# Optimization experiments

Measured on AMD Instinct MI355X. Metric: run time of the kernel, lower is better.

## Reference

```python
import jax, jax.numpy as jnp
import numpy as np

N, L, D_IN = 8192, 32, 256   # total paths, max path len, token+method embed
E, H, T, C = 128, 128, 128, 2  # encode_size, hidden_dim, test_vector_size, label_count
G = 1024                      # number of methods (groups)
LN_EPS = 1e-5


def _lstm_last_hidden(xs, lengths, Wih, Whh, bih, bhh):
    """Single-layer LSTM over padded [N,L,E]; returns h at t=length-1 per row (packed-sequence h_n)."""
    xs_t = jnp.transpose(xs, (1, 0, 2))  # [L, N, E]
    n = xs.shape[0]
    h0 = jnp.zeros((n, H), xs.dtype)
    c0 = jnp.zeros((n, H), xs.dtype)

    def step(carry, inp):
        h, c = carry
        x_t, t = inp
        gates = x_t @ Wih.T + bih + h @ Whh.T + bhh  # [N, 4H], torch gate order i,f,g,o
        i, f, g, o = jnp.split(gates, 4, axis=-1)
        c_new = jax.nn.sigmoid(f) * c + jax.nn.sigmoid(i) * jnp.tanh(g)
        h_new = jax.nn.sigmoid(o) * jnp.tanh(c_new)
        valid = (t < lengths)[:, None]  # freeze state past each path's length
        return (jnp.where(valid, h_new, h), jnp.where(valid, c_new, c)), None

    (h_last, _), _ = jax.lax.scan(step, (h0, c0), (xs_t, jnp.arange(L)))
    return h_last  # [N, H]


def setup_inputs() -> dict:
    key = jax.random.key(0)
    ks = jax.random.split(key, 10)
    rng = np.random.default_rng(0)

    inputs = jax.random.normal(ks[0], (N, L, D_IN), dtype=jnp.float32)
    path_lengths = jnp.asarray(rng.integers(1, L + 1, size=N), dtype=jnp.int32)
    # sorted segment ids, every group non-empty (torch.split groups are contiguous and >=1)
    ids = np.sort(np.concatenate([np.arange(G), rng.integers(0, G, size=N - G)]))
    segment_ids = jnp.asarray(ids, dtype=jnp.int32)

    s = 0.05
    W_in = jax.random.normal(ks[1], (E, D_IN), dtype=jnp.float32) * s
    ln_gamma = jnp.ones((E,), jnp.float32)
    ln_beta = jnp.zeros((E,), jnp.float32)
    Wih = jax.random.normal(ks[2], (4 * H, E), dtype=jnp.float32) * s
    Whh = jax.random.normal(ks[3], (4 * H, H), dtype=jnp.float32) * s
    bih = jax.random.normal(ks[4], (4 * H,), dtype=jnp.float32) * s
    bhh = jax.random.normal(ks[5], (4 * H,), dtype=jnp.float32) * s
    attn_param = jax.random.normal(ks[6], (H,), dtype=jnp.float32) * s
    W_out = jax.random.normal(ks[7], (T, H), dtype=jnp.float32) * s
    W_cls = jax.random.normal(ks[8], (C, T), dtype=jnp.float32) * s

    return {"inputs": inputs, "path_lengths": path_lengths, "segment_ids": segment_ids,
            "W_in": W_in, "ln_gamma": ln_gamma, "ln_beta": ln_beta,
            "Wih": Wih, "Whh": Whh, "bih": bih, "bhh": bhh,
            "attn_param": attn_param, "W_out": W_out, "W_cls": W_cls}


def reference(inputs, path_lengths, segment_ids, W_in, ln_gamma, ln_beta,
              Wih, Whh, bih, bhh, attn_param, W_out, W_cls):
    # input projection + layernorm + tanh (dropout disabled, p=0)
    x = inputs @ W_in.T  # [N, L, E]
    mu = jnp.mean(x, axis=-1, keepdims=True)
    var = jnp.mean((x - mu) ** 2, axis=-1, keepdims=True)
    x = jnp.tanh((x - mu) * jax.lax.rsqrt(var + LN_EPS) * ln_gamma + ln_beta)

    h = _lstm_last_hidden(x, path_lengths, Wih, Whh, bih, bhh)  # [N, H]

    # segmented softmax attention + mean over each group's paths
    logits = h @ attn_param  # [N]
    m = jax.ops.segment_max(logits, segment_ids, num_segments=G)
    e = jnp.exp(logits - m[segment_ids])
    Z = jax.ops.segment_sum(e, segment_ids, num_segments=G)
    attn = e / Z[segment_ids]  # per-group softmax weights
    wsum = jax.ops.segment_sum(attn[:, None] * h, segment_ids, num_segments=G)  # [G, H]
    counts = jax.ops.segment_sum(jnp.ones_like(logits), segment_ids, num_segments=G)
    code = wsum / counts[:, None]  # torch.mean divides by group size

    code_vectors = code @ W_out.T  # [G, T]
    outputs = code_vectors @ W_cls.T  # [G, C]
    return outputs, code_vectors, attn_param
```

## Files before the change

kernel.cpp:

```cpp
#include <hip/hip_runtime.h>


#define NPATH 8192
#define LMAX  32
#define DIN   256
#define EDIM  128
#define HDIM  128
#define NGRP  1024
#define NTOK  (NPATH * LMAX)
#define NCHUNK 512
#define XSLAB ((long)NPATH * EDIM)
#define K1_TILE 64
#define K1_TPB  16

typedef __attribute__((ext_vector_type(8))) short short8;
typedef __attribute__((ext_vector_type(4))) short s16x4;
typedef __attribute__((ext_vector_type(4))) float f32x4;

__device__ __forceinline__ unsigned short f2bf(float f) {
    unsigned int x = __float_as_uint(f);
    x += 0x7fffu + ((x >> 16) & 1u);
    return (unsigned short)(x >> 16);
}
__device__ __forceinline__ float sigmoid_f(float x) {
    return __fdividef(1.f, 1.f + __expf(-x));
}
__device__ __forceinline__ float tanh_f(float x) {
    float t = __expf(-2.f * x);
    return __fdividef(2.f, 1.f + t) - 1.f;
}

__global__ __launch_bounds__(512) void k0_sort(const int* __restrict__ lens,
                                               int* __restrict__ perm,
                                               int* __restrict__ inv) {
    __shared__ int hw[8][LMAX];
    __shared__ int startg[8][LMAX];
    __shared__ int colsum[LMAX];
    __shared__ int binoff[LMAX];
    const int tid = threadIdx.x;
    const int w = tid >> 6, lane = tid & 63;
    if (lane < LMAX) hw[w][lane] = 0;
    __syncthreads();
    for (int i = tid; i < NPATH; i += 512)
        atomicAdd(&hw[w][lens[i] - 1], 1);
    __syncthreads();
    if (tid < LMAX) {
        int s = 0;
        #pragma unroll
        for (int ww = 0; ww < 8; ++ww) { startg[ww][tid] = s; s += hw[ww][tid]; }
        colsum[tid] = s;
    }
    __syncthreads();
    if (tid == 0) {
        int s = 0;
        for (int b = 0; b < LMAX; ++b) { binoff[b] = s; s += colsum[b]; }
    }
    __syncthreads();
    if (tid < LMAX) {
        #pragma unroll
        for (int ww = 0; ww < 8; ++ww) startg[ww][tid] += binoff[tid];
    }
    __syncthreads();
    for (int i = tid; i < NPATH; i += 512) {
        int b = lens[i] - 1;
        int p = atomicAdd(&startg[w][b], 1);
        perm[p] = i;
        inv[i] = p;
    }
}

__global__ __launch_bounds__(512, 2) void k1_proj(
    const float* __restrict__ inp, const float* __restrict__ Win,
    const float* __restrict__ gam, const float* __restrict__ bet,
    const int* __restrict__ inv, unsigned short* __restrict__ xt)
{
    __shared__ unsigned short Bs[EDIM * DIN];
    __shared__ unsigned short As[2][K1_TILE * DIN];
    __shared__ float lnx[2][K1_TILE][2];
    const int tid = threadIdx.x;
    const int w = tid >> 6, lane = tid & 63, q = lane >> 4, c = lane & 15;
    const int rg = w >> 1, ch = w & 1;
    const int xr = (c & 7) << 3;

    {
        const int row = tid >> 2, c0 = (tid & 3) * 64;
        const float* src = Win + row * DIN + c0;
        const int key = (row & 7) << 3;
        #pragma unroll
        for (int j = 0; j < 8; ++j) {
            float4 u0 = *(const float4*)(src + j * 8);
            float4 u1 = *(const float4*)(src + j * 8 + 4);
            short8 s;
            s[0] = (short)f2bf(u0.x); s[1] = (short)f2bf(u0.y);
            s[2] = (short)f2bf(u0.z); s[3] = (short)f2bf(u0.w);
            s[4] = (short)f2bf(u1.x); s[5] = (short)f2bf(u1.y);
            s[6] = (short)f2bf(u1.z); s[7] = (short)f2bf(u1.w);
            *(short8*)&Bs[row * DIN + ((c0 + j * 8) ^ key)] = s;
        }
    }

    const int arow = tid >> 3, ac0 = (tid & 7) * 32;
    const int akey = (arow & 7) << 3;
    const long tile0 = (long)blockIdx.x * K1_TPB;

    float gr[4], br[4];
    #pragma unroll
    for (int i = 0; i < 4; ++i) {
        int col = ch * 64 + i * 16 + c;
        gr[i] = gam[col]; br[i] = bet[col];
    }

    {
        const float* src = inp + (tile0 * K1_TILE + arow) * DIN + ac0;
        #pragma unroll
        for (int j = 0; j < 4; ++j) {
            float4 u0 = *(const float4*)(src + j * 8);
            float4 u1 = *(const float4*)(src + j * 8 + 4);
            short8 s;
            s[0] = (short)f2bf(u0.x); s[1] = (short)f2bf(u0.y);
            s[2] = (short)f2bf(u0.z); s[3] = (short)f2bf(u0.w);
            s[4] = (short)f2bf(u1.x); s[5] = (short)f2bf(u1.y);
            s[6] = (short)f2bf(u1.z); s[7] = (short)f2bf(u1.w);
            *(short8*)&As[0][arow * DIN + ((ac0 + j * 8) ^ akey)] = s;
        }
    }
    __syncthreads();

    for (int it = 0; it < K1_TPB; ++it) {
        const int cur = it & 1, nxt = cur ^ 1;
        unsigned short* Acur = &As[0][0] + cur * (K1_TILE * DIN);
        unsigned short* Anxt = &As[0][0] + nxt * (K1_TILE * DIN);

        float4 fr[8];
        if (it + 1 < K1_TPB) {
            const float* src = inp + ((tile0 + it + 1) * K1_TILE + arow) * DIN + ac0;
            #pragma unroll
            for (int j = 0; j < 8; ++j) fr[j] = *(const float4*)(src + j * 4);
        }

        f32x4 acc[4];
        const f32x4 fzero = {0.f, 0.f, 0.f, 0.f};
        #pragma unroll
        for (int i = 0; i < 4; ++i) acc[i] = fzero;
        const unsigned short* arow_p = &Acur[(rg * 16 + c) * DIN];
        #pragma unroll
        for (int ks = 0; ks < 8; ++ks) {
            short8 a = *(const short8*)(arow_p + ((q * 8 + ks * 32) ^ xr));
            #pragma unroll
            for (int i = 0; i < 4; ++i) {
                short8 b = *(const short8*)&Bs[(ch * 64 + i * 16 + c) * DIN
                                               + ((q * 8 + ks * 32) ^ xr)];
                acc[i] = __builtin_amdgcn_mfma_f32_16x16x32_bf16(a, b, acc[i], 0, 0, 0);
            }
        }

        float sr[4], qr[4];
        #pragma unroll
        for (int r = 0; r < 4; ++r) {
            float s = 0.f, ss = 0.f;
            #pragma unroll
            for (int i = 0; i < 4; ++i) { float v = acc[i][r]; s += v; ss += v * v; }
            #pragma unroll
            for (int m = 1; m < 16; m <<= 1) { s += __shfl_xor(s, m, 64); ss += __shfl_xor(ss, m, 64); }
            sr[r] = s; qr[r] = ss;
            if (c == 0) { lnx[ch][rg * 16 + q * 4 + r][0] = s; lnx[ch][rg * 16 + q * 4 + r][1] = ss; }
        }
        __syncthreads();

        #pragma unroll
        for (int r = 0; r < 4; ++r) {
            const int grow = rg * 16 + q * 4 + r;
            float s = sr[r] + lnx[ch ^ 1][grow][0];
            float ss = qr[r] + lnx[ch ^ 1][grow][1];
            float mu = s * (1.f / 128.f);
            float rstd = rsqrtf(ss * (1.f / 128.f) - mu * mu + 1e-5f);
            const int key = (grow & 7) << 3;
            #pragma unroll
            for (int i = 0; i < 4; ++i) {
                float v = (acc[i][r] - mu) * rstd * gr[i] + br[i];
                Acur[grow * DIN + ((ch * 64 + i * 16 + c) ^ key)] = f2bf(tanh_f(v));
            }
        }

        if (it + 1 < K1_TPB) {
            #pragma unroll
            for (int j = 0; j < 4; ++j) {
                float4 u0 = fr[j * 2], u1 = fr[j * 2 + 1];
                short8 s;
                s[0] = (short)f2bf(u0.x); s[1] = (short)f2bf(u0.y);
                s[2] = (short)f2bf(u0.z); s[3] = (short)f2bf(u0.w);
                s[4] = (short)f2bf(u1.x); s[5] = (short)f2bf(u1.y);
                s[6] = (short)f2bf(u1.z); s[7] = (short)f2bf(u1.w);
                *(short8*)&Anxt[arow * DIN + ((ac0 + j * 8) ^ akey)] = s;
            }
        }
        __syncthreads();

        {
            const int row = tid >> 3, e0 = (tid & 7) * 16;
            const int key = (row & 7) << 3;
            short8 v0 = *(const short8*)&Acur[row * DIN + (e0 ^ key)];
            short8 v1 = *(const short8*)&Acur[row * DIN + ((e0 + 8) ^ key)];
            const long m = (tile0 + it) * K1_TILE + row;
            const int path = (int)(m >> 5), t = (int)(m & 31);
            const int slot = inv[path];
            unsigned short* dst = &xt[(long)t * XSLAB + (long)slot * EDIM + e0];
            *(short8*)dst = v0;
            *(short8*)(dst + 8) = v1;
        }
    }
}

__global__ __launch_bounds__(512, 2) void k2_lstm(
    const unsigned short* __restrict__ xt,
    const float* __restrict__ Wih, const float* __restrict__ Whh,
    const float* __restrict__ bih, const float* __restrict__ bhh,
    const int* __restrict__ lens, const int* __restrict__ perm,
    float* __restrict__ h_last)
{
    __shared__ unsigned short wih_s[512 * 128];
    __shared__ unsigned short hb[2][16 * 128];
    __shared__ unsigned short xb[2][16 * 128];
    __shared__ int pemb[16];
    __shared__ int lenb[16];
    const int tid = threadIdx.x;
    const int w = tid >> 6, lane = tid & 63, q = lane >> 4, c = lane & 15;
    const int xr = (c & 7) << 3;

    #pragma unroll
    for (int i = 0; i < 32; ++i) {
        int chunk = i * 512 + tid;
        int j = chunk >> 5, c4 = chunk & 31;
        float4 v = *(const float4*)&Wih[j * EDIM + c4 * 4];
        s16x4 s = { (short)f2bf(v.x), (short)f2bf(v.y), (short)f2bf(v.z), (short)f2bf(v.w) };
        *(s16x4*)&wih_s[j * 128 + ((c4 * 4) ^ ((j & 7) << 3))] = s;
    }

    short8 whf[4][4];
    float bs[4];
    #pragma unroll
    for (int g = 0; g < 4; ++g) {
        const int j = g * 128 + w * 16 + c;
        bs[g] = bih[j] + bhh[j];
        const float* ph = Whh + (long)j * HDIM + q * 8;
        #pragma unroll
        for (int ks = 0; ks < 4; ++ks) {
            float4 b0 = *(const float4*)(ph + ks * 32);
            float4 b1 = *(const float4*)(ph + ks * 32 + 4);
            short8 u;
            u[0] = (short)f2bf(b0.x); u[1] = (short)f2bf(b0.y);
            u[2] = (short)f2bf(b0.z); u[3] = (short)f2bf(b0.w);
            u[4] = (short)f2bf(b1.x); u[5] = (short)f2bf(b1.y);
            u[6] = (short)f2bf(b1.z); u[7] = (short)f2bf(b1.w);
            whf[g][ks] = u;
        }
    }

    int koff[4];
    #pragma unroll
    for (int ks = 0; ks < 4; ++ks) koff[ks] = (q * 8 + ks * 32) ^ xr;
    const unsigned short* wbase[4];
    #pragma unroll
    for (int g = 0; g < 4; ++g) wbase[g] = &wih_s[(g * 128 + w * 16 + c) * 128];

    const int srow = tid >> 5;
    const int scol = (tid * 4) & 127;
    const int sdst = srow * 128 + (scol ^ ((srow & 7) << 3));

    for (int half = 0; half < 2; ++half) {
        const int cid = half ? (NCHUNK - 1 - (int)blockIdx.x) : (int)blockIdx.x;
        const int r0 = cid * 16;
        if (tid < 16) { int p = perm[r0 + tid]; pemb[tid] = p; lenb[tid] = lens[p]; }
        { s16x4 z = {0, 0, 0, 0}; *(s16x4*)&hb[0][tid * 4] = z; }
        {
            s16x4 v = *(const s16x4*)&xt[(long)r0 * EDIM + tid * 4];
            *(s16x4*)&xb[0][sdst] = v;
        }
        __syncthreads();

        int steps = 1;
        #pragma unroll
        for (int i = 0; i < 16; ++i) steps = (lenb[i] > steps) ? lenb[i] : steps;
        int lenr[4];
        #pragma unroll
        for (int r = 0; r < 4; ++r) lenr[r] = lenb[q * 4 + r];

        float c_reg[4] = {0.f, 0.f, 0.f, 0.f};
        float h_reg[4] = {0.f, 0.f, 0.f, 0.f};

        int cur = 0;
        for (int t = 0; t < steps; ++t) {
            const int tn = (t + 1 < steps) ? (t + 1) : t;
            s16x4 xg = *(const s16x4*)&xt[(long)tn * XSLAB + (long)r0 * EDIM + tid * 4];

            f32x4 acc[4];
            #pragma unroll
            for (int g = 0; g < 4; ++g) {
                f32x4 a = {bs[g], bs[g], bs[g], bs[g]};
                acc[g] = a;
            }
            if (t) {
                short8 ha[4];
                #pragma unroll
                for (int ks = 0; ks < 4; ++ks)
                    ha[ks] = *(const short8*)&hb[cur][c * 128 + koff[ks]];
                #pragma unroll
                for (int ks = 0; ks < 4; ++ks)
                    #pragma unroll
                    for (int g = 0; g < 4; ++g)
                        acc[g] = __builtin_amdgcn_mfma_f32_16x16x32_bf16(ha[ks], whf[g][ks], acc[g], 0, 0, 0);
            }
            #pragma unroll
            for (int ks = 0; ks < 4; ++ks) {
                short8 xa = *(const short8*)&xb[cur][c * 128 + koff[ks]];
                #pragma unroll
                for (int g = 0; g < 4; ++g) {
                    short8 b = *(const short8*)(wbase[g] + koff[ks]);
                    acc[g] = __builtin_amdgcn_mfma_f32_16x16x32_bf16(xa, b, acc[g], 0, 0, 0);
                }
            }
            const int nxt = cur ^ 1;
            *(s16x4*)&xb[nxt][sdst] = xg;

            #pragma unroll
            for (int r = 0; r < 4; ++r) {
                float cn = sigmoid_f(acc[1][r]) * c_reg[r]
                         + sigmoid_f(acc[0][r]) * tanh_f(acc[2][r]);
                float hn = sigmoid_f(acc[3][r]) * tanh_f(cn);
                if (t < lenr[r]) { c_reg[r] = cn; h_reg[r] = hn; }
                const int row = q * 4 + r;
                hb[nxt][row * 128 + ((w * 16 + c) ^ ((row & 7) << 3))] = f2bf(h_reg[r]);
            }
            __syncthreads();
            cur = nxt;
        }
        #pragma unroll
        for (int r = 0; r < 4; ++r)
            h_last[(long)pemb[q * 4 + r] * HDIM + w * 16 + c] = h_reg[r];
        if (half == 0) __syncthreads();
    }
}

__global__ __launch_bounds__(64) void k3_attn(
    const float* __restrict__ h_last, const int* __restrict__ seg,
    const float* __restrict__ attn, const float* __restrict__ Wout,
    const float* __restrict__ Wcls, float* __restrict__ out)
{
    __shared__ float code_s[128];
    const int g = blockIdx.x, l = threadIdx.x;

    int lo, hi;
    { int a = 0, b = NPATH; while (a < b) { int m = (a + b) >> 1; if (seg[m] < g) a = m + 1; else b = m; } lo = a; }
    { int a = lo, b = NPATH; while (a < b) { int m = (a + b) >> 1; if (seg[m] < g + 1) a = m + 1; else b = m; } hi = a; }

    float a0 = attn[l], a1 = attn[l + 64];
    float mrun = -1e30f, Z = 0.f;
    for (int n = lo; n < hi; ++n) {
        const float* hr = &h_last[(long)n * HDIM];
        float v = hr[l] * a0 + hr[l + 64] * a1;
        #pragma unroll
        for (int m = 1; m < 64; m <<= 1) v += __shfl_xor(v, m, 64);
        float nm = fmaxf(mrun, v);
        Z = Z * __expf(mrun - nm) + __expf(v - nm);
        mrun = nm;
    }
    float w0 = 0.f, w1 = 0.f;
    for (int n = lo; n < hi; ++n) {
        const float* hr = &h_last[(long)n * HDIM];
        float v = hr[l] * a0 + hr[l + 64] * a1;
        #pragma unroll
        for (int m = 1; m < 64; m <<= 1) v += __shfl_xor(v, m, 64);
        float at = __expf(v - mrun) / Z;
        w0 += at * hr[l]; w1 += at * hr[l + 64];
    }
    float inv_cnt = (hi > lo) ? 1.f / (float)(hi - lo) : 0.f;
    code_s[l] = w0 * inv_cnt; code_s[l + 64] = w1 * inv_cnt;
    __syncthreads();

    float cv0 = 0.f, cv1 = 0.f;
    for (int k = 0; k < 128; ++k) {
        float ck = code_s[k];
        cv0 += ck * Wout[l * 128 + k];
        cv1 += ck * Wout[(l + 64) * 128 + k];
    }
    out[2048 + g * 128 + l]      = cv0;
    out[2048 + g * 128 + l + 64] = cv1;

    float p0 = cv0 * Wcls[l] + cv1 * Wcls[l + 64];
    float p1 = cv0 * Wcls[128 + l] + cv1 * Wcls[128 + l + 64];
    #pragma unroll
    for (int m = 1; m < 64; m <<= 1) { p0 += __shfl_xor(p0, m, 64); p1 += __shfl_xor(p1, m, 64); }
    if (l == 0) { out[g * 2 + 0] = p0; out[g * 2 + 1] = p1; }
    if (g == 0) { out[133120 + l] = attn[l]; out[133120 + 64 + l] = attn[l + 64]; }
}

extern "C" void kernel_launch(void* const* d_in, const int* in_sizes, int n_in,
                              void* d_out, int out_size, void* d_ws, size_t ws_size,
                              hipStream_t stream) {
    const float* inp  = (const float*)d_in[0];
    const int*   lens = (const int*)d_in[1];
    const int*   seg  = (const int*)d_in[2];
    const float* Win  = (const float*)d_in[3];
    const float* gam  = (const float*)d_in[4];
    const float* bet  = (const float*)d_in[5];
    const float* Wih  = (const float*)d_in[6];
    const float* Whh  = (const float*)d_in[7];
    const float* bih  = (const float*)d_in[8];
    const float* bhh  = (const float*)d_in[9];
    const float* attn = (const float*)d_in[10];
    const float* Wout = (const float*)d_in[11];
    const float* Wcls = (const float*)d_in[12];

    unsigned short* xt = (unsigned short*)d_ws;
    float* h_last = (float*)((char*)d_ws + (size_t)NTOK * EDIM * 2);
    int* perm = (int*)((char*)d_ws + (size_t)NTOK * EDIM * 2
                                   + (size_t)NPATH * HDIM * 4);
    int* inv  = perm + NPATH;

    hipLaunchKernelGGL(k0_sort, dim3(1), dim3(512), 0, stream, lens, perm, inv);
    hipLaunchKernelGGL(k1_proj, dim3(256), dim3(512), 0, stream, inp, Win, gam, bet, inv, xt);
    hipLaunchKernelGGL(k2_lstm, dim3(NCHUNK / 2), dim3(512), 0, stream,
                       xt, Wih, Whh, bih, bhh, lens, perm, h_last);
    hipLaunchKernelGGL(k3_attn, dim3(NGRP), dim3(64), 0, stream, h_last, seg, attn, Wout, Wcls,
                       (float*)d_out);
}
```

Baseline: 541.4 us.

## Process 32 sorted paths per LSTM block with register-resident Wih halves

The LSTM kernel now gives each block one 32-row chunk instead of two sequential 16-row chunks. Each B fragment (Whh and Wih) is reused across two M tiles, which halves weight fetches per MFMA. Half of Wih (gates g,o) is held in registers and the other half sits in LDS with a new k-blocked layout, so the LDS footprint drops. The step count now comes from the last sorted row's length (lenb[31]), which assumes the permutation sorts paths by ascending length within each chunk. The two halves of work per block are no longer length-balanced, and register pressure rises.

```diff
diff --git a/kernel.cpp b/kernel.cpp
--- a/kernel.cpp
+++ b/kernel.cpp
@@ -8,10 +8,10 @@
 #define HDIM  128
 #define NGRP  1024
 #define NTOK  (NPATH * LMAX)
-#define NCHUNK 512
 #define XSLAB ((long)NPATH * EDIM)
 #define K1_TILE 64
 #define K1_TPB  16
+#define NCH32 256
 
 typedef __attribute__((ext_vector_type(8))) short short8;
 typedef __attribute__((ext_vector_type(4))) short s16x4;
@@ -218,25 +218,25 @@
     const int* __restrict__ lens, const int* __restrict__ perm,
     float* __restrict__ h_last)
 {
-    __shared__ unsigned short wih_s[512 * 128];
-    __shared__ unsigned short hb[2][16 * 128];
-    __shared__ unsigned short xb[2][16 * 128];
-    __shared__ int pemb[16];
-    __shared__ int lenb[16];
+    __shared__ unsigned short wih2[16 * 256 * 8];
+    __shared__ unsigned short hb2[2][16 * 32 * 8];
+    __shared__ unsigned short xb2[2][16 * 32 * 8];
+    __shared__ int pemb[32];
+    __shared__ int lenb[32];
     const int tid = threadIdx.x;
     const int w = tid >> 6, lane = tid & 63, q = lane >> 4, c = lane & 15;
-    const int xr = (c & 7) << 3;
-
-    #pragma unroll
-    for (int i = 0; i < 32; ++i) {
+
+    #pragma unroll
+    for (int i = 0; i < 16; ++i) {
         int chunk = i * 512 + tid;
-        int j = chunk >> 5, c4 = chunk & 31;
-        float4 v = *(const float4*)&Wih[j * EDIM + c4 * 4];
+        int j2 = chunk >> 5, c4 = chunk & 31;
+        float4 v = *(const float4*)&Wih[j2 * EDIM + c4 * 4];
         s16x4 s = { (short)f2bf(v.x), (short)f2bf(v.y), (short)f2bf(v.z), (short)f2bf(v.w) };
-        *(s16x4*)&wih_s[j * 128 + ((c4 * 4) ^ ((j & 7) << 3))] = s;
+        *(s16x4*)&wih2[((c4 >> 1) * 256 + j2) * 8 + (c4 & 1) * 4] = s;
     }
 
     short8 whf[4][4];
+    short8 wfv[2][4];
     float bs[4];
     #pragma unroll
     for (int g = 0; g < 4; ++g) {
@@ -255,90 +255,107 @@
             whf[g][ks] = u;
         }
     }
-
-    int koff[4];
-    #pragma unroll
-    for (int ks = 0; ks < 4; ++ks) koff[ks] = (q * 8 + ks * 32) ^ xr;
-    const unsigned short* wbase[4];
-    #pragma unroll
-    for (int g = 0; g < 4; ++g) wbase[g] = &wih_s[(g * 128 + w * 16 + c) * 128];
-
-    const int srow = tid >> 5;
-    const int scol = (tid * 4) & 127;
-    const int sdst = srow * 128 + (scol ^ ((srow & 7) << 3));
-
-    for (int half = 0; half < 2; ++half) {
-        const int cid = half ? (NCHUNK - 1 - (int)blockIdx.x) : (int)blockIdx.x;
-        const int r0 = cid * 16;
-        if (tid < 16) { int p = perm[r0 + tid]; pemb[tid] = p; lenb[tid] = lens[p]; }
-        { s16x4 z = {0, 0, 0, 0}; *(s16x4*)&hb[0][tid * 4] = z; }
-        {
-            s16x4 v = *(const s16x4*)&xt[(long)r0 * EDIM + tid * 4];
-            *(s16x4*)&xb[0][sdst] = v;
-        }
-        __syncthreads();
-
-        int steps = 1;
-        #pragma unroll
-        for (int i = 0; i < 16; ++i) steps = (lenb[i] > steps) ? lenb[i] : steps;
-        int lenr[4];
-        #pragma unroll
-        for (int r = 0; r < 4; ++r) lenr[r] = lenb[q * 4 + r];
-
-        float c_reg[4] = {0.f, 0.f, 0.f, 0.f};
-        float h_reg[4] = {0.f, 0.f, 0.f, 0.f};
-
-        int cur = 0;
-        for (int t = 0; t < steps; ++t) {
-            const int tn = (t + 1 < steps) ? (t + 1) : t;
-            s16x4 xg = *(const s16x4*)&xt[(long)tn * XSLAB + (long)r0 * EDIM + tid * 4];
-
-            f32x4 acc[4];
+    #pragma unroll
+    for (int gi = 0; gi < 2; ++gi) {
+        const int j = (2 + gi) * 128 + w * 16 + c;
+        const float* pi = Wih + (long)j * EDIM + q * 8;
+        #pragma unroll
+        for (int ks = 0; ks < 4; ++ks) {
+            float4 a0 = *(const float4*)(pi + ks * 32);
+            float4 a1 = *(const float4*)(pi + ks * 32 + 4);
+            short8 s;
+            s[0] = (short)f2bf(a0.x); s[1] = (short)f2bf(a0.y);
+            s[2] = (short)f2bf(a0.z); s[3] = (short)f2bf(a0.w);
+            s[4] = (short)f2bf(a1.x); s[5] = (short)f2bf(a1.y);
+            s[6] = (short)f2bf(a1.z); s[7] = (short)f2bf(a1.w);
+            wfv[gi][ks] = s;
+        }
+    }
+
+    const int r0 = blockIdx.x * 32;
+    if (tid < 32) { int p = perm[r0 + tid]; pemb[tid] = p; lenb[tid] = lens[p]; }
+    const int srow = tid >> 4, skb = tid & 15;
+    const int sdst = (skb * 32 + srow) * 8;
+    {
+        short8 v = *(const short8*)&xt[(long)(r0 + srow) * EDIM + skb * 8];
+        *(short8*)&xb2[0][sdst] = v;
+    }
+    __syncthreads();
+
+    const int steps = lenb[31];
+    int lenr[2][4];
+    #pragma unroll
+    for (int m = 0; m < 2; ++m)
+        #pragma unroll
+        for (int r = 0; r < 4; ++r) lenr[m][r] = lenb[m * 16 + q * 4 + r];
+
+    float c_reg[2][4] = {{0.f,0.f,0.f,0.f},{0.f,0.f,0.f,0.f}};
+    float h_reg[2][4] = {{0.f,0.f,0.f,0.f},{0.f,0.f,0.f,0.f}};
+
+    int cur = 0;
+    for (int t = 0; t < steps; ++t) {
+        const int tn = (t + 1 < steps) ? (t + 1) : t;
+        short8 xg = *(const short8*)&xt[(long)tn * XSLAB + (long)(r0 + srow) * EDIM + skb * 8];
+
+        f32x4 acc[2][4];
+        #pragma unroll
+        for (int m = 0; m < 2; ++m)
             #pragma unroll
             for (int g = 0; g < 4; ++g) {
                 f32x4 a = {bs[g], bs[g], bs[g], bs[g]};
-                acc[g] = a;
-            }
-            if (t) {
-                short8 ha[4];
-                #pragma unroll
-                for (int ks = 0; ks < 4; ++ks)
-                    ha[ks] = *(const short8*)&hb[cur][c * 128 + koff[ks]];
-                #pragma unroll
-                for (int ks = 0; ks < 4; ++ks)
-                    #pragma unroll
-                    for (int g = 0; g < 4; ++g)
-                        acc[g] = __builtin_amdgcn_mfma_f32_16x16x32_bf16(ha[ks], whf[g][ks], acc[g], 0, 0, 0);
-            }
+                acc[m][g] = a;
+            }
+        if (t) {
             #pragma unroll
             for (int ks = 0; ks < 4; ++ks) {
-                short8 xa = *(const short8*)&xb[cur][c * 128 + koff[ks]];
+                short8 ha0 = *(const short8*)&hb2[cur][((q + 4 * ks) * 32 + c) * 8];
+                short8 ha1 = *(const short8*)&hb2[cur][((q + 4 * ks) * 32 + 16 + c) * 8];
                 #pragma unroll
                 for (int g = 0; g < 4; ++g) {
-                    short8 b = *(const short8*)(wbase[g] + koff[ks]);
-                    acc[g] = __builtin_amdgcn_mfma_f32_16x16x32_bf16(xa, b, acc[g], 0, 0, 0);
+                    acc[0][g] = __builtin_amdgcn_mfma_f32_16x16x32_bf16(ha0, whf[g][ks], acc[0][g], 0, 0, 0);
+                    acc[1][g] = __builtin_amdgcn_mfma_f32_16x16x32_bf16(ha1, whf[g][ks], acc[1][g], 0, 0, 0);
                 }
             }
-            const int nxt = cur ^ 1;
-            *(s16x4*)&xb[nxt][sdst] = xg;
-
+        }
+        #pragma unroll
+        for (int ks = 0; ks < 4; ++ks) {
+            short8 xa0 = *(const short8*)&xb2[cur][((q + 4 * ks) * 32 + c) * 8];
+            short8 xa1 = *(const short8*)&xb2[cur][((q + 4 * ks) * 32 + 16 + c) * 8];
+            short8 b0 = *(const short8*)&wih2[((q + 4 * ks) * 256 + w * 16 + c) * 8];
+            short8 b1 = *(const short8*)&wih2[((q + 4 * ks) * 256 + 128 + w * 16 + c) * 8];
+            acc[0][0] = __builtin_amdgcn_mfma_f32_16x16x32_bf16(xa0, b0, acc[0][0], 0, 0, 0);
+            acc[1][0] = __builtin_amdgcn_mfma_f32_16x16x32_bf16(xa1, b0, acc[1][0], 0, 0, 0);
+            acc[0][1] = __builtin_amdgcn_mfma_f32_16x16x32_bf16(xa0, b1, acc[0][1], 0, 0, 0);
+            acc[1][1] = __builtin_amdgcn_mfma_f32_16x16x32_bf16(xa1, b1, acc[1][1], 0, 0, 0);
+            acc[0][2] = __builtin_amdgcn_mfma_f32_16x16x32_bf16(xa0, wfv[0][ks], acc[0][2], 0, 0, 0);
+            acc[1][2] = __builtin_amdgcn_mfma_f32_16x16x32_bf16(xa1, wfv[0][ks], acc[1][2], 0, 0, 0);
+            acc[0][3] = __builtin_amdgcn_mfma_f32_16x16x32_bf16(xa0, wfv[1][ks], acc[0][3], 0, 0, 0);
+            acc[1][3] = __builtin_amdgcn_mfma_f32_16x16x32_bf16(xa1, wfv[1][ks], acc[1][3], 0, 0, 0);
+        }
+        const int nxt = cur ^ 1;
+        *(short8*)&xb2[nxt][sdst] = xg;
+
+        #pragma unroll
+        for (int m = 0; m < 2; ++m)
             #pragma unroll
             for (int r = 0; r < 4; ++r) {
-                float cn = sigmoid_f(acc[1][r]) * c_reg[r]
-                         + sigmoid_f(acc[0][r]) * tanh_f(acc[2][r]);
-                float hn = sigmoid_f(acc[3][r]) * tanh_f(cn);
-                if (t < lenr[r]) { c_reg[r] = cn; h_reg[r] = hn; }
-                const int row = q * 4 + r;
-                hb[nxt][row * 128 + ((w * 16 + c) ^ ((row & 7) << 3))] = f2bf(h_reg[r]);
-            }
-            __syncthreads();
-            cur = nxt;
-        }
+                float cn = sigmoid_f(acc[m][1][r]) * c_reg[m][r]
+                         + sigmoid_f(acc[m][0][r]) * tanh_f(acc[m][2][r]);
+                float hn = sigmoid_f(acc[m][3][r]) * tanh_f(cn);
+                if (t < lenr[m][r]) { c_reg[m][r] = cn; h_reg[m][r] = hn; }
+                const int row = m * 16 + q * 4 + r;
+                const int kb = w * 2 + (c >> 3);
+                hb2[nxt][(kb * 32 + row) * 8 + (c & 7)] = f2bf(h_reg[m][r]);
+            }
+        __syncthreads();
+        cur = nxt;
+    }
+
+    #pragma unroll
+    for (int m = 0; m < 2; ++m)
         #pragma unroll
         for (int r = 0; r < 4; ++r)
-            h_last[(long)pemb[q * 4 + r] * HDIM + w * 16 + c] = h_reg[r];
-        if (half == 0) __syncthreads();
-    }
+            h_last[(long)pemb[m * 16 + q * 4 + r] * HDIM + w * 16 + c] = h_reg[m][r];
 }
 
 __global__ __launch_bounds__(64) void k3_attn(
@@ -419,7 +436,7 @@
 
     hipLaunchKernelGGL(k0_sort, dim3(1), dim3(512), 0, stream, lens, perm, inv);
     hipLaunchKernelGGL(k1_proj, dim3(256), dim3(512), 0, stream, inp, Win, gam, bet, inv, xt);
-    hipLaunchKernelGGL(k2_lstm, dim3(NCHUNK / 2), dim3(512), 0, stream,
+    hipLaunchKernelGGL(k2_lstm, dim3(NCH32), dim3(512), 0, stream,
                        xt, Wih, Whh, bih, bhh, lens, perm, h_last);
     hipLaunchKernelGGL(k3_attn, dim3(NGRP), dim3(64), 0, stream, h_last, seg, attn, Wout, Wcls,
                        (float*)d_out);
```

Result: slower. 587.1 us (+8.4%).

## Restructure LSTM LDS layouts, keep half of Wih in registers, use raw exp/rcp

Applied to the files above, without the earlier changes.

Replaces the XOR-swizzled row-major LDS buffers for Wih, h and x with a k-blocked layout, so each MFMA operand fetch becomes a contiguous 16-byte read. Half of the Wih gate slices (the g and o gates) move into registers, which halves Wih LDS traffic and footprint. It also switches sigmoid/tanh to raw v_exp_f32/v_rcp_f32 asm and takes the step count from the last (longest) sorted row. In exchange it adds 32 VGPRs per thread under a 512x2 launch bound, which risks spills. It also drops the clamp on the next-step prefetch, so it reads one slab past the end of xt when a chunk runs all 32 steps.

```diff
diff --git a/kernel.cpp b/kernel.cpp
--- a/kernel.cpp
+++ b/kernel.cpp
@@ -8,10 +8,10 @@
 #define HDIM  128
 #define NGRP  1024
 #define NTOK  (NPATH * LMAX)
-#define NCHUNK 512
 #define XSLAB ((long)NPATH * EDIM)
 #define K1_TILE 64
 #define K1_TPB  16
+#define NCHUNK 512
 
 typedef __attribute__((ext_vector_type(8))) short short8;
 typedef __attribute__((ext_vector_type(4))) short s16x4;
@@ -22,12 +22,18 @@
     x += 0x7fffu + ((x >> 16) & 1u);
     return (unsigned short)(x >> 16);
 }
+__device__ __forceinline__ float exp2_f(float x) {
+    float r; asm("v_exp_f32 %0, %1" : "=v"(r) : "v"(x)); return r;
+}
+__device__ __forceinline__ float rcp_f(float x) {
+    float r; asm("v_rcp_f32 %0, %1" : "=v"(r) : "v"(x)); return r;
+}
+#define L2E 1.4426950408889634f
 __device__ __forceinline__ float sigmoid_f(float x) {
-    return __fdividef(1.f, 1.f + __expf(-x));
+    return rcp_f(1.f + exp2_f(-L2E * x));
 }
 __device__ __forceinline__ float tanh_f(float x) {
-    float t = __expf(-2.f * x);
-    return __fdividef(2.f, 1.f + t) - 1.f;
+    return 2.f * rcp_f(1.f + exp2_f(-2.f * L2E * x)) - 1.f;
 }
 
 __global__ __launch_bounds__(512) void k0_sort(const int* __restrict__ lens,
@@ -218,25 +224,25 @@
     const int* __restrict__ lens, const int* __restrict__ perm,
     float* __restrict__ h_last)
 {
-    __shared__ unsigned short wih_s[512 * 128];
-    __shared__ unsigned short hb[2][16 * 128];
-    __shared__ unsigned short xb[2][16 * 128];
+    __shared__ unsigned short wih2[16 * 256 * 8];
+    __shared__ unsigned short hb2[2][16 * 16 * 8];
+    __shared__ unsigned short xb2[2][16 * 16 * 8];
     __shared__ int pemb[16];
     __shared__ int lenb[16];
     const int tid = threadIdx.x;
     const int w = tid >> 6, lane = tid & 63, q = lane >> 4, c = lane & 15;
-    const int xr = (c & 7) << 3;
 
     #pragma unroll
-    for (int i = 0; i < 32; ++i) {
+    for (int i = 0; i < 16; ++i) {
         int chunk = i * 512 + tid;
-        int j = chunk >> 5, c4 = chunk & 31;
-        float4 v = *(const float4*)&Wih[j * EDIM + c4 * 4];
+        int j2 = chunk >> 5, c4 = chunk & 31;
+        float4 v = *(const float4*)&Wih[j2 * EDIM + c4 * 4];
         s16x4 s = { (short)f2bf(v.x), (short)f2bf(v.y), (short)f2bf(v.z), (short)f2bf(v.w) };
-        *(s16x4*)&wih_s[j * 128 + ((c4 * 4) ^ ((j & 7) << 3))] = s;
+        *(s16x4*)&wih2[((c4 >> 1) * 256 + j2) * 8 + (c4 & 1) * 4] = s;
     }
 
     short8 whf[4][4];
+    short8 wfv[2][4];
     float bs[4];
     #pragma unroll
     for (int g = 0; g < 4; ++g) {
@@ -255,32 +261,37 @@
             whf[g][ks] = u;
         }
     }
-
-    int koff[4];
     #pragma unroll
-    for (int ks = 0; ks < 4; ++ks) koff[ks] = (q * 8 + ks * 32) ^ xr;
-    const unsigned short* wbase[4];
-    #pragma unroll
-    for (int g = 0; g < 4; ++g) wbase[g] = &wih_s[(g * 128 + w * 16 + c) * 128];
-
-    const int srow = tid >> 5;
-    const int scol = (tid * 4) & 127;
-    const int sdst = srow * 128 + (scol ^ ((srow & 7) << 3));
+    for (int gi = 0; gi < 2; ++gi) {
+        const int j = (2 + gi) * 128 + w * 16 + c;
+        const float* pi = Wih + (long)j * EDIM + q * 8;
+        #pragma unroll
+        for (int ks = 0; ks < 4; ++ks) {
+            float4 a0 = *(const float4*)(pi + ks * 32);
+            float4 a1 = *(const float4*)(pi + ks * 32 + 4);
+            short8 s;
+            s[0] = (short)f2bf(a0.x); s[1] = (short)f2bf(a0.y);
+            s[2] = (short)f2bf(a0.z); s[3] = (short)f2bf(a0.w);
+            s[4] = (short)f2bf(a1.x); s[5] = (short)f2bf(a1.y);
+            s[6] = (short)f2bf(a1.z); s[7] = (short)f2bf(a1.w);
+            wfv[gi][ks] = s;
+        }
+    }
+
+    const int srow = tid >> 5, squad = tid & 31;
+    const int sdst = ((squad >> 1) * 16 + srow) * 8 + (squad & 1) * 4;
+    const int hkb = w * 2 + (c >> 3), hsub = c & 7;
 
     for (int half = 0; half < 2; ++half) {
         const int cid = half ? (NCHUNK - 1 - (int)blockIdx.x) : (int)blockIdx.x;
         const int r0 = cid * 16;
         if (tid < 16) { int p = perm[r0 + tid]; pemb[tid] = p; lenb[tid] = lens[p]; }
-        { s16x4 z = {0, 0, 0, 0}; *(s16x4*)&hb[0][tid * 4] = z; }
-        {
-            s16x4 v = *(const s16x4*)&xt[(long)r0 * EDIM + tid * 4];
-            *(s16x4*)&xb[0][sdst] = v;
-        }
+        { s16x4 z = {0, 0, 0, 0}; *(s16x4*)&hb2[0][tid * 4] = z; }
+        const unsigned short* xsrc = &xt[(long)(r0 + srow) * EDIM + squad * 4];
+        { s16x4 v = *(const s16x4*)xsrc; *(s16x4*)&xb2[0][sdst] = v; }
         __syncthreads();
 
-        int steps = 1;
-        #pragma unroll
-        for (int i = 0; i < 16; ++i) steps = (lenb[i] > steps) ? lenb[i] : steps;
+        const int steps = lenb[15];
         int lenr[4];
         #pragma unroll
         for (int r = 0; r < 4; ++r) lenr[r] = lenb[q * 4 + r];
@@ -289,9 +300,10 @@
         float h_reg[4] = {0.f, 0.f, 0.f, 0.f};
 
         int cur = 0;
+        const unsigned short* xp = xsrc;
         for (int t = 0; t < steps; ++t) {
-            const int tn = (t + 1 < steps) ? (t + 1) : t;
-            s16x4 xg = *(const s16x4*)&xt[(long)tn * XSLAB + (long)r0 * EDIM + tid * 4];
+            xp += XSLAB;
+            s16x4 xg = *(const s16x4*)xp;
 
             f32x4 acc[4];
             #pragma unroll
@@ -300,27 +312,26 @@
                 acc[g] = a;
             }
             if (t) {
-                short8 ha[4];
                 #pragma unroll
-                for (int ks = 0; ks < 4; ++ks)
-                    ha[ks] = *(const short8*)&hb[cur][c * 128 + koff[ks]];
-                #pragma unroll
-                for (int ks = 0; ks < 4; ++ks)
+                for (int ks = 0; ks < 4; ++ks) {
+                    short8 ha = *(const short8*)&hb2[cur][((q + 4 * ks) * 16 + c) * 8];
                     #pragma unroll
                     for (int g = 0; g < 4; ++g)
-                        acc[g] = __builtin_amdgcn_mfma_f32_16x16x32_bf16(ha[ks], whf[g][ks], acc[g], 0, 0, 0);
+                        acc[g] = __builtin_amdgcn_mfma_f32_16x16x32_bf16(ha, whf[g][ks], acc[g], 0, 0, 0);
+                }
             }
             #pragma unroll
             for (int ks = 0; ks < 4; ++ks) {
-                short8 xa = *(const short8*)&xb[cur][c * 128 + koff[ks]];
-                #pragma unroll
-                for (int g = 0; g < 4; ++g) {
-                    short8 b = *(const short8*)(wbase[g] + koff[ks]);
-                    acc[g] = __builtin_amdgcn_mfma_f32_16x16x32_bf16(xa, b, acc[g], 0, 0, 0);
-                }
+                short8 xa = *(const short8*)&xb2[cur][((q + 4 * ks) * 16 + c) * 8];
+                short8 b0 = *(const short8*)&wih2[((q + 4 * ks) * 256 + w * 16 + c) * 8];
+                short8 b1 = *(const short8*)&wih2[((q + 4 * ks) * 256 + 128 + w * 16 + c) * 8];
+                acc[0] = __builtin_amdgcn_mfma_f32_16x16x32_bf16(xa, b0, acc[0], 0, 0, 0);
+                acc[1] = __builtin_amdgcn_mfma_f32_16x16x32_bf16(xa, b1, acc[1], 0, 0, 0);
+                acc[2] = __builtin_amdgcn_mfma_f32_16x16x32_bf16(xa, wfv[0][ks], acc[2], 0, 0, 0);
+                acc[3] = __builtin_amdgcn_mfma_f32_16x16x32_bf16(xa, wfv[1][ks], acc[3], 0, 0, 0);
             }
             const int nxt = cur ^ 1;
-            *(s16x4*)&xb[nxt][sdst] = xg;
+            *(s16x4*)&xb2[nxt][sdst] = xg;
 
             #pragma unroll
             for (int r = 0; r < 4; ++r) {
@@ -329,7 +340,7 @@
                 float hn = sigmoid_f(acc[3][r]) * tanh_f(cn);
                 if (t < lenr[r]) { c_reg[r] = cn; h_reg[r] = hn; }
                 const int row = q * 4 + r;
-                hb[nxt][row * 128 + ((w * 16 + c) ^ ((row & 7) << 3))] = f2bf(h_reg[r]);
+                hb2[nxt][(hkb * 16 + row) * 8 + hsub] = f2bf(h_reg[r]);
             }
             __syncthreads();
             cur = nxt;
```

Measured after the change: 498.2 us. 1.09x faster.
